# Kernel optimization log

Hardware: AMD Instinct MI355X
Metric: run time of the kernel (lower is better)

Reference implementation:

```python
import jax, jax.numpy as jnp
import numpy as np


def _mish(x):
    return x * jnp.tanh(jax.nn.softplus(x))


def setup_inputs() -> dict:
    key = jax.random.key(0)
    ks = jax.random.split(key, 10)
    N, D, U, NB, M, MD = 2048, 1024, 2048, 4, 8192, 1024
    g = lambda k, shape, s=0.02: jax.random.normal(k, shape, jnp.float32) * s
    return dict(
        x=jax.random.normal(ks[0], (N, D), jnp.float32),
        w=g(ks[1], (D, U, NB)),
        delay=g(ks[2], (D, U, NB)),
        b=jnp.zeros((U, NB), jnp.float32),
        gate_W=g(ks[3], (D, NB)),
        gate_b=jnp.zeros((NB,), jnp.float32),
        neuron_avg=jax.random.uniform(ks[4], (U,), jnp.float32),
        conn_W1=g(ks[5], (U, 32)),
        conn_b1=jnp.zeros((32,), jnp.float32),
        conn_W2=g(ks[6], (32, U)),
        conn_b2=jnp.zeros((U,), jnp.float32),
        mask=jnp.ones((U,), jnp.float32),
        act_w=jnp.ones((9,), jnp.float32),
        read_W=g(ks[7], (U, M)),
        read_b=jnp.zeros((M,), jnp.float32),
        memory=g(ks[8], (M, MD), 1.0),
    )


def reference(x, w, delay, b, gate_W, gate_b, neuron_avg, conn_W1, conn_b1,
              conn_W2, conn_b2, mask, act_w, read_W, read_b, memory):
    # --- DynamicPlasticDenseDendritic forward ---
    w_mod = w * jax.nn.sigmoid(delay)                      # [D,U,NB]
    branch = jnp.einsum('nd,dub->nub', x, w_mod) + b       # [N,U,NB]
    gate = jax.nn.softmax(x @ gate_W + gate_b, axis=-1)    # [N,NB]
    z = jnp.einsum('nub,nb->nu', branch, gate)             # [N,U]
    # DynamicConnectivity on neuron activation averages (single row)
    h = jax.nn.relu(neuron_avg[None, :] @ conn_W1 + conn_b1)   # [1,32]
    conn = jax.nn.sigmoid(h @ conn_W2 + conn_b2)               # [1,U]
    a = jax.nn.relu(z * conn * mask[None, :])                  # [N,U]
    # --- LearnedActivation: softmax-weighted 8-way activation blend (+zero) ---
    wts = jax.nn.softmax(act_w)
    blend = (wts[0] * jax.nn.sigmoid(a) + wts[1] * jax.nn.elu(a)
             + wts[2] * jnp.tanh(a) + wts[3] * jax.nn.relu(a)
             + wts[4] * jax.nn.silu(a) + wts[5] * jax.nn.gelu(a, approximate=False)
             + wts[6] * jax.nn.selu(a) + wts[7] * _mish(a))
    # --- EpisodicMemory read ---
    attn = jax.nn.softmax(blend @ read_W + read_b, axis=-1)   # [N,M]
    read = attn @ memory                                       # [N,MD]
    return read
```

## Files before the change

kernel.cpp:

```cpp
#include <hip/hip_runtime.h>


typedef unsigned short u16;
typedef __attribute__((ext_vector_type(8))) short bf16x8;
typedef __attribute__((ext_vector_type(4))) float f32x4;

__device__ __forceinline__ float b2f(u16 h) {
    union { unsigned u; float f; } v; v.u = ((unsigned)h) << 16; return v.f;
}
__device__ __forceinline__ u16 f2b(float f) {
    union { float f; unsigned u; } v; v.f = f;
    unsigned u = v.u;
    return (u16)((u + 0x7fffu + ((u >> 16) & 1u)) >> 16);
}

__device__ __forceinline__ void async_copy16(void* lds, const void* g) {
    __builtin_amdgcn_global_load_lds(
        (__attribute__((address_space(1))) void*)(g),
        (__attribute__((address_space(3))) void*)(lds), 16, 0, 0);
}

template<int BM, int BN, int S>
__device__ __forceinline__ void gemm_core_db(const u16* __restrict__ A,
                                             const u16* __restrict__ B,
                                             int Kloop, int ld,
                                             int row0, int col0,
                                             u16* smem,
                                             f32x4 (&acc)[BM / 32][BN / 32])
{
    constexpr int MT = BM / 32, NT = BN / 32;
    constexpr int STG = (BM + BN) * 32;
    constexpr int SET = STG * S;
    const int tid  = threadIdx.x;
    const int lane = tid & 63;
    const int wv   = tid >> 6;
    const int wr   = wv >> 1, wc = wv & 1;
    const int lr   = lane & 15, kg = lane >> 4;

#pragma unroll
    for (int i = 0; i < MT; i++)
#pragma unroll
        for (int j = 0; j < NT; j++) {
            f32x4 z = {0.f, 0.f, 0.f, 0.f};
            acc[i][j] = z;
        }

    auto stage_in = [&](u16* set, int k0) {
#pragma unroll
        for (int c = tid; c < BM * 4; c += 256) {
            const u16* gA = A + (size_t)(row0 + (c >> 2)) * ld + k0 + (c & 3) * 8;
#pragma unroll
            for (int s = 0; s < S; s++)
                async_copy16(set + s * STG + c * 8, gA + s * 32);
        }
#pragma unroll
        for (int c = tid; c < BN * 4; c += 256) {
            const u16* gB = B + (size_t)(col0 + (c >> 2)) * ld + k0 + (c & 3) * 8;
#pragma unroll
            for (int s = 0; s < S; s++)
                async_copy16(set + s * STG + BM * 32 + c * 8, gB + s * 32);
        }
    };

    stage_in(smem, 0);
    __syncthreads();

    int p = 0;
    for (int k0 = 0; k0 < Kloop; k0 += 32 * S) {
        if (k0 + 32 * S < Kloop)
            stage_in(smem + (p ^ 1) * SET, k0 + 32 * S);
        u16* set = smem + p * SET;
#pragma unroll
        for (int s = 0; s < S; s++) {
            const u16* sA = set + s * STG;
            const u16* sB = sA + BM * 32;
            bf16x8 af[MT], bfr[NT];
#pragma unroll
            for (int i = 0; i < MT; i++)
                af[i] = *(const bf16x8*)(sA + ((wr * (BM / 2) + i * 16 + lr) * 32 + kg * 8));
#pragma unroll
            for (int j = 0; j < NT; j++)
                bfr[j] = *(const bf16x8*)(sB + ((wc * (BN / 2) + j * 16 + lr) * 32 + kg * 8));
#pragma unroll
            for (int i = 0; i < MT; i++)
#pragma unroll
                for (int j = 0; j < NT; j++)
                    acc[i][j] = __builtin_amdgcn_mfma_f32_16x16x32_bf16(
                                    af[i], bfr[j], acc[i][j], 0, 0, 0);
        }
        __syncthreads();
        p ^= 1;
    }
}

__global__ __launch_bounds__(256)
void k_small(const float* __restrict__ na, const float* __restrict__ W1,
             const float* __restrict__ b1, const float* __restrict__ W2,
             const float* __restrict__ b2, const float* __restrict__ actw,
             float* __restrict__ conn, float* __restrict__ wts)
{
    __shared__ float red[256 * 32];
    __shared__ float hsh[32];
    const int tid = threadIdx.x;
    float h[32];
#pragma unroll
    for (int k = 0; k < 32; k++) h[k] = 0.f;
    for (int u = tid; u < 2048; u += 256) {
        float nav = na[u];
        const float* row = W1 + u * 32;
#pragma unroll
        for (int k = 0; k < 32; k++) h[k] += nav * row[k];
    }
#pragma unroll
    for (int k = 0; k < 32; k++) red[tid * 32 + k] = h[k];
    for (int s = 128; s > 0; s >>= 1) {
        __syncthreads();
        if (tid < s)
#pragma unroll
            for (int k = 0; k < 32; k++) red[tid * 32 + k] += red[(tid + s) * 32 + k];
    }
    __syncthreads();
    if (tid < 32) hsh[tid] = fmaxf(red[tid] + b1[tid], 0.f);
    if (tid == 0) {
        float e[9], m = -1e30f;
        for (int i = 0; i < 9; i++) { e[i] = actw[i]; m = fmaxf(m, e[i]); }
        float s = 0.f;
        for (int i = 0; i < 9; i++) { e[i] = expf(e[i] - m); s += e[i]; }
        for (int i = 0; i < 9; i++) wts[i] = e[i] / s;
    }
    __syncthreads();
    for (int u = tid; u < 2048; u += 256) {
        float a = 0.f;
#pragma unroll
        for (int k = 0; k < 32; k++) a += hsh[k] * W2[k * 2048 + u];
        conn[u] = 1.f / (1.f + expf(-(a + b2[u])));
    }
}

__global__ __launch_bounds__(256)
void k_gate_y(const float* __restrict__ x, const float* __restrict__ gW,
              const float* __restrict__ gb, float* __restrict__ gate,
              u16* __restrict__ y)
{
    const int tid = threadIdx.x, lane = tid & 63, wv = tid >> 6;
    const int n = blockIdx.x * 4 + wv;
    const float* xr = x + (size_t)n * 1024;
    float a0 = 0, a1 = 0, a2 = 0, a3 = 0;
    float xv[16];
#pragma unroll
    for (int s = 0; s < 16; s++) {
        int d = s * 64 + lane;
        float xd = xr[d]; xv[s] = xd;
        float4 g4 = *(const float4*)(gW + d * 4);
        a0 += xd * g4.x; a1 += xd * g4.y; a2 += xd * g4.z; a3 += xd * g4.w;
    }
#pragma unroll
    for (int off = 32; off > 0; off >>= 1) {
        a0 += __shfl_xor(a0, off); a1 += __shfl_xor(a1, off);
        a2 += __shfl_xor(a2, off); a3 += __shfl_xor(a3, off);
    }
    a0 += gb[0]; a1 += gb[1]; a2 += gb[2]; a3 += gb[3];
    float m = fmaxf(fmaxf(a0, a1), fmaxf(a2, a3));
    float e0 = expf(a0 - m), e1 = expf(a1 - m), e2 = expf(a2 - m), e3 = expf(a3 - m);
    float inv = 1.f / (e0 + e1 + e2 + e3);
    float g0 = e0 * inv, g1 = e1 * inv, g2 = e2 * inv, g3 = e3 * inv;
    if (lane == 0) *(float4*)(gate + n * 4) = make_float4(g0, g1, g2, g3);
#pragma unroll
    for (int s = 0; s < 16; s++) {
        int d = s * 64 + lane;
        ushort4 o;
        o.x = f2b(xv[s] * g0); o.y = f2b(xv[s] * g1);
        o.z = f2b(xv[s] * g2); o.w = f2b(xv[s] * g3);
        *(ushort4*)(y + (size_t)n * 4096 + d * 4) = o;
    }
}

__global__ __launch_bounds__(256)
void k_wmT(const float* __restrict__ w, const float* __restrict__ delay,
           u16* __restrict__ wmT)
{
    __shared__ __align__(16) ushort4 tile[32][65];
    const int tid = threadIdx.x;
    const int tx = tid & 63, ty = tid >> 6;
    const int u0 = blockIdx.x * 64, d0 = blockIdx.y * 32;
#pragma unroll
    for (int i = 0; i < 8; i++) {
        int d = i * 4 + ty;
        size_t idx = ((size_t)(d0 + d) * 2048 + (u0 + tx)) * 4;
        float4 w4 = *(const float4*)(w + idx);
        float4 d4 = *(const float4*)(delay + idx);
        ushort4 o;
        o.x = f2b(w4.x / (1.f + expf(-d4.x)));
        o.y = f2b(w4.y / (1.f + expf(-d4.y)));
        o.z = f2b(w4.z / (1.f + expf(-d4.z)));
        o.w = f2b(w4.w / (1.f + expf(-d4.w)));
        tile[d][tx] = o;
    }
    __syncthreads();
    const int dx = tid & 31, uy = tid >> 5;
#pragma unroll
    for (int i = 0; i < 8; i++) {
        int u = i * 8 + uy;
        *(ushort4*)(wmT + (size_t)(u0 + u) * 4096 + (d0 + dx) * 4) = tile[dx][u];
    }
}

__global__ __launch_bounds__(256)
void k_transpose(const float* __restrict__ in, u16* __restrict__ out, int R, int C)
{
    __shared__ __align__(16) u16 t[64][68];
    const int tid = threadIdx.x, tx = tid & 15, ty = tid >> 4;
    const int c0 = blockIdx.x * 64, r0 = blockIdx.y * 64;
#pragma unroll
    for (int i = 0; i < 4; i++) {
        int r = r0 + ty + i * 16;
        float4 v = *(const float4*)(in + (size_t)r * C + c0 + tx * 4);
        t[tx * 4 + 0][ty + i * 16] = f2b(v.x); t[tx * 4 + 1][ty + i * 16] = f2b(v.y);
        t[tx * 4 + 2][ty + i * 16] = f2b(v.z); t[tx * 4 + 3][ty + i * 16] = f2b(v.w);
    }
    __syncthreads();
#pragma unroll
    for (int i = 0; i < 4; i++) {
        int c = ty + i * 16;
        ushort4 v;
        v.x = t[c][tx * 4 + 0]; v.y = t[c][tx * 4 + 1];
        v.z = t[c][tx * 4 + 2]; v.w = t[c][tx * 4 + 3];
        *(ushort4*)(out + (size_t)(c0 + c) * R + r0 + tx * 4) = v;
    }
}

__device__ __forceinline__ float act_blend(float a,
    float w0, float w1, float w2, float w3,
    float w4, float w5, float w6, float w7)
{
    float sig = 1.f / (1.f + expf(-a));
    float elu = (a > 0.f) ? a : (expf(a) - 1.f);
    float th  = tanhf(a);
    float rel = fmaxf(a, 0.f);
    float sil = a * sig;
    float gel = a * 0.5f * (1.f + erff(a * 0.70710678118654752f));
    float sel = (a > 0.f) ? 1.0507009873554805f * a
                          : 1.0507009873554805f * 1.6732632423543772f * (expf(a) - 1.f);
    float sp  = (a > 20.f) ? a : log1pf(expf(a));
    float mish = a * tanhf(sp);
    return w0 * sig + w1 * elu + w2 * th + w3 * rel + w4 * sil + w5 * gel
         + w6 * sel + w7 * mish;
}

template<int BM, int BN, int NCOL>
__global__ __launch_bounds__(256, 4)
void k_gemm_partial(const u16* __restrict__ A, const u16* __restrict__ B,
                    int Kchunk, int ld, float* __restrict__ P)
{
    constexpr int MT = BM / 32, NT = BN / 32;
    __shared__ __align__(16) u16 smem[2 * (BM + BN) * 32];

    const int nx = gridDim.x, ny = gridDim.y;
    const int f  = blockIdx.x + nx * blockIdx.y;
    const int ch = (nx * ny) >> 3;
    const int sw = (f & 7) * ch + (f >> 3);
    const int bx = sw % nx, by = sw / nx;
    const int row0 = by * BM, col0 = bx * BN;

    const u16* Ac = A + (size_t)blockIdx.z * Kchunk;
    const u16* Bc = B + (size_t)blockIdx.z * Kchunk;

    f32x4 acc[MT][NT];
    gemm_core_db<BM, BN, 1>(Ac, Bc, Kchunk, ld, row0, col0, smem, acc);

    float* Pz = P + (size_t)blockIdx.z * 2048 * NCOL;
    const int tid = threadIdx.x, lane = tid & 63, wv = tid >> 6;
    const int wr = wv >> 1, wc = wv & 1, lr = lane & 15, kg = lane >> 4;
#pragma unroll
    for (int i = 0; i < MT; i++)
#pragma unroll
        for (int r = 0; r < 4; r++) {
            int n = row0 + wr * (BM / 2) + i * 16 + kg * 4 + r;
            size_t ob = (size_t)n * NCOL;
#pragma unroll
            for (int j = 0; j < NT; j++)
                Pz[ob + col0 + wc * (BN / 2) + j * 16 + lr] = acc[i][j][r];
        }
}

__global__ __launch_bounds__(256)
void k_reduce_blend(const float* __restrict__ P, const float* __restrict__ gate,
                    const float* __restrict__ conn, const float* __restrict__ mask,
                    const float* __restrict__ wts, const float* __restrict__ bbias,
                    u16* __restrict__ blend)
{
    constexpr size_t SL = (size_t)2048 * 2048;
    const int n  = blockIdx.x;
    const int u0 = threadIdx.x * 8;
    const float* base = P + (size_t)n * 2048 + u0;

    float v[8];
#pragma unroll
    for (int h = 0; h < 2; h++) {
        float4 a = *(const float4*)(base + h * 4);
        float4 b = *(const float4*)(base + SL + h * 4);
        float4 c = *(const float4*)(base + 2 * SL + h * 4);
        float4 d = *(const float4*)(base + 3 * SL + h * 4);
        v[h * 4 + 0] = a.x + b.x + c.x + d.x;
        v[h * 4 + 1] = a.y + b.y + c.y + d.y;
        v[h * 4 + 2] = a.z + b.z + c.z + d.z;
        v[h * 4 + 3] = a.w + b.w + c.w + d.w;
    }
    float4 g = *(const float4*)(gate + n * 4);
    const float w0 = wts[0], w1 = wts[1], w2 = wts[2], w3 = wts[3];
    const float w4 = wts[4], w5 = wts[5], w6 = wts[6], w7 = wts[7];

    ushort4 o[2];
#pragma unroll
    for (int j = 0; j < 8; j++) {
        int u = u0 + j;
        float4 b4 = *(const float4*)(bbias + u * 4);
        float z = v[j] + g.x * b4.x + g.y * b4.y + g.z * b4.z + g.w * b4.w;
        float a = fmaxf(z * conn[u] * mask[u], 0.f);
        u16 r = f2b(act_blend(a, w0, w1, w2, w3, w4, w5, w6, w7));
        ((u16*)o)[j] = r;
    }
    *(ushort4*)(blend + (size_t)n * 2048 + u0)     = o[0];
    *(ushort4*)(blend + (size_t)n * 2048 + u0 + 4) = o[1];
}

__global__ __launch_bounds__(256, 2)
void k_gemm_logits(const u16* __restrict__ BL, const u16* __restrict__ RWT,
                   const float* __restrict__ rbias, u16* __restrict__ out)
{
    __shared__ __align__(16) u16 smem[2 * (128 + 128) * 32];
    const int nx = gridDim.x, ny = gridDim.y;
    const int f  = blockIdx.x + nx * blockIdx.y;
    const int ch = (nx * ny) >> 3;
    const int sw = (f & 7) * ch + (f >> 3);
    const int bx = sw % nx, by = sw / nx;

    f32x4 acc[4][4];
    const int row0 = by * 128, col0 = bx * 128;
    gemm_core_db<128, 128, 1>(BL, RWT, 2048, 2048, row0, col0, smem, acc);

    const int tid = threadIdx.x, lane = tid & 63, wv = tid >> 6;
    const int wr = wv >> 1, wc = wv & 1, lr = lane & 15, kg = lane >> 4;
    float rb[4]; int mm[4];
#pragma unroll
    for (int j = 0; j < 4; j++) {
        mm[j] = col0 + wc * 64 + j * 16 + lr;
        rb[j] = rbias[mm[j]];
    }
#pragma unroll
    for (int i = 0; i < 4; i++)
#pragma unroll
        for (int r = 0; r < 4; r++) {
            int n = row0 + wr * 64 + i * 16 + kg * 4 + r;
            size_t ob = (size_t)n * 8192;
#pragma unroll
            for (int j = 0; j < 4; j++)
                out[ob + mm[j]] = f2b(acc[i][j][r] + rb[j]);
        }
}

__global__ __launch_bounds__(256)
void k_softmax(u16* __restrict__ buf)
{
    __shared__ float red[8];
    const int tid = threadIdx.x, lane = tid & 63, wv = tid >> 6;
    u16* row = buf + (size_t)blockIdx.x * 8192;
    float v[32];
    float mx = -1e30f;
#pragma unroll
    for (int s = 0; s < 8; s++) {
        ushort4 u4 = *(const ushort4*)(row + (s * 256 + tid) * 4);
        float a = b2f(u4.x), b = b2f(u4.y), c = b2f(u4.z), d = b2f(u4.w);
        v[s * 4 + 0] = a; v[s * 4 + 1] = b; v[s * 4 + 2] = c; v[s * 4 + 3] = d;
        mx = fmaxf(mx, fmaxf(fmaxf(a, b), fmaxf(c, d)));
    }
#pragma unroll
    for (int off = 32; off > 0; off >>= 1) mx = fmaxf(mx, __shfl_xor(mx, off));
    if (lane == 0) red[wv] = mx;
    __syncthreads();
    mx = fmaxf(fmaxf(red[0], red[1]), fmaxf(red[2], red[3]));
    float sum = 0.f;
#pragma unroll
    for (int k = 0; k < 32; k++) { v[k] = expf(v[k] - mx); sum += v[k]; }
#pragma unroll
    for (int off = 32; off > 0; off >>= 1) sum += __shfl_xor(sum, off);
    if (lane == 0) red[4 + wv] = sum;
    __syncthreads();
    float inv = 1.f / (red[4] + red[5] + red[6] + red[7]);
#pragma unroll
    for (int s = 0; s < 8; s++) {
        ushort4 o;
        o.x = f2b(v[s * 4 + 0] * inv); o.y = f2b(v[s * 4 + 1] * inv);
        o.z = f2b(v[s * 4 + 2] * inv); o.w = f2b(v[s * 4 + 3] * inv);
        *(ushort4*)(row + (s * 256 + tid) * 4) = o;
    }
}

__global__ __launch_bounds__(256)
void k_reduce_out(const float* __restrict__ P, float* __restrict__ out)
{
    constexpr size_t SL = (size_t)2048 * 1024;
    size_t i = ((size_t)blockIdx.x * 256 + threadIdx.x) * 4;
    float4 a = *(const float4*)(P + i);
    float4 b = *(const float4*)(P + SL + i);
    float4 c = *(const float4*)(P + 2 * SL + i);
    float4 d = *(const float4*)(P + 3 * SL + i);
    float4 o;
    o.x = a.x + b.x + c.x + d.x;
    o.y = a.y + b.y + c.y + d.y;
    o.z = a.z + b.z + c.z + d.z;
    o.w = a.w + b.w + c.w + d.w;
    *(float4*)(out + i) = o;
}

__global__ void k_fill(float* out, int n)
{
    int i = blockIdx.x * 256 + threadIdx.x;
    if (i < n) out[i] = 12345.f;
}

extern "C" void kernel_launch(void* const* d_in, const int* in_sizes, int n_in,
                              void* d_out, int out_size, void* d_ws, size_t ws_size,
                              hipStream_t stream)
{
    const float* x     = (const float*)d_in[0];
    const float* w     = (const float*)d_in[1];
    const float* delay = (const float*)d_in[2];
    const float* bb    = (const float*)d_in[3];
    const float* gW    = (const float*)d_in[4];
    const float* gb    = (const float*)d_in[5];
    const float* na    = (const float*)d_in[6];
    const float* cW1   = (const float*)d_in[7];
    const float* cb1   = (const float*)d_in[8];
    const float* cW2   = (const float*)d_in[9];
    const float* cb2   = (const float*)d_in[10];
    const float* mask  = (const float*)d_in[11];
    const float* actw  = (const float*)d_in[12];
    const float* rW    = (const float*)d_in[13];
    const float* rb    = (const float*)d_in[14];
    const float* mem   = (const float*)d_in[15];
    (void)in_sizes; (void)n_in;

    char* ws = (char*)d_ws;
    size_t off = 0;
    auto alloc = [&](size_t bytes) {
        size_t o = off; off += (bytes + 255) & ~(size_t)255; return o;
    };
    size_t o_wts   = alloc(9 * 4);
    size_t o_gate  = alloc(2048 * 4 * 4);
    size_t o_conn  = alloc(2048 * 4);
    size_t o_y     = alloc((size_t)2048 * 4096 * 2);
    size_t o_wmT   = alloc((size_t)2048 * 4096 * 2);
    size_t o_blend = alloc((size_t)2048 * 2048 * 2);
    size_t o_rwT   = alloc((size_t)8192 * 2048 * 2);
    size_t o_log   = alloc((size_t)2048 * 8192 * 2);

    if (off > ws_size) {
        k_fill<<<(out_size + 255) / 256, 256, 0, stream>>>((float*)d_out, out_size);
        return;
    }

    float* wts   = (float*)(ws + o_wts);
    float* gate  = (float*)(ws + o_gate);
    float* conn  = (float*)(ws + o_conn);
    u16* y       = (u16*)(ws + o_y);
    u16* wmT     = (u16*)(ws + o_wmT);
    u16* blend   = (u16*)(ws + o_blend);
    u16* rwT     = (u16*)(ws + o_rwT);
    u16* logits  = (u16*)(ws + o_log);
    u16* memT    = y;

    float* pA = (float*)(ws + o_rwT);
    float* pC = (float*)(ws + o_rwT);

    k_small<<<1, 256, 0, stream>>>(na, cW1, cb1, cW2, cb2, actw, conn, wts);
    k_gate_y<<<512, 256, 0, stream>>>(x, gW, gb, gate, y);
    k_wmT<<<dim3(32, 32), 256, 0, stream>>>(w, delay, wmT);

    k_gemm_partial<128, 128, 2048><<<dim3(16, 16, 4), 256, 0, stream>>>(
        y, wmT, 1024, 4096, pA);
    k_reduce_blend<<<2048, 256, 0, stream>>>(pA, gate, conn, mask, wts, bb, blend);

    k_transpose<<<dim3(128, 32), 256, 0, stream>>>(rW, rwT, 2048, 8192);
    k_gemm_logits<<<dim3(64, 16), 256, 0, stream>>>(blend, rwT, rb, logits);
    k_softmax<<<2048, 256, 0, stream>>>(logits);

    k_transpose<<<dim3(16, 128), 256, 0, stream>>>(mem, memT, 8192, 1024);

    k_gemm_partial<128, 128, 1024><<<dim3(8, 16, 4), 256, 0, stream>>>(
        logits, memT, 2048, 8192, pC);
    k_reduce_out<<<2048, 256, 0, stream>>>(pC, (float*)d_out);
}
```

Before: 484.8 us.

## Use 256x256 eight-wave GEMM core with swizzled LDS for first two GEMMs

Adds a new 512-thread GEMM core that computes 256x256 output tiles with BK=64, double-buffered LDS staging via global_load_lds, an XOR swizzle against bank conflicts, and interleaved LDS reads and MFMA phases using s_setprio. The branch GEMM and the logits GEMM now use this core in place of the 128x128 four-wave kernel. Larger tiles give more operand reuse per LDS byte and fewer global loads. The cost is 128KB of LDS per block and fewer blocks (256 for each GEMM), which may underfill the GPU's CUs and lower occupancy.

```diff
diff --git a/kernel.cpp b/kernel.cpp
--- a/kernel.cpp
+++ b/kernel.cpp
@@ -18,6 +18,133 @@
     __builtin_amdgcn_global_load_lds(
         (__attribute__((address_space(1))) void*)(g),
         (__attribute__((address_space(3))) void*)(lds), 16, 0, 0);
+}
+
+__device__ __forceinline__ int swz(int o) { return o ^ (((o >> 9) & 1) << 5); }
+
+__device__ __forceinline__ void stage_tile256(const u16* __restrict__ src, int ld,
+                                              int base0, int k0,
+                                              char* ldsbase, int tid)
+{
+#pragma unroll
+    for (int h = 0; h < 2; h++)
+#pragma unroll
+        for (int it = 0; it < 2; it++) {
+            int o = it * 8192 + tid * 16;
+            int s = swz(o);
+            int r = s >> 7;
+            int c = (s & 127) >> 1;
+            async_copy16(ldsbase + h * 16384 + o,
+                         src + (size_t)(base0 + h * 128 + r) * ld + k0 + c);
+        }
+}
+
+__device__ __forceinline__ void gemm256_core8(const u16* __restrict__ A,
+                                              const u16* __restrict__ B,
+                                              int Ktiles, int ld,
+                                              int row0, int col0,
+                                              char* lds, f32x4 (&acc)[8][4])
+{
+    const int tid  = threadIdx.x;
+    const int lane = tid & 63;
+    const int wv   = tid >> 6;
+    const int wr   = wv >> 2;
+    const int wc   = wv & 3;
+    const int lr   = lane & 15, kg = lane >> 4;
+
+#pragma unroll
+    for (int i = 0; i < 8; i++)
+#pragma unroll
+        for (int j = 0; j < 4; j++) {
+            f32x4 z = {0.f, 0.f, 0.f, 0.f};
+            acc[i][j] = z;
+        }
+
+    stage_tile256(A, ld, row0, 0, lds, tid);
+    stage_tile256(B, ld, col0, 0, lds + 32768, tid);
+    asm volatile("s_waitcnt vmcnt(0)" ::: "memory");
+    __builtin_amdgcn_s_barrier();
+
+    bf16x8 af[4][2], bfr[2][2];
+
+    for (int t = 0; t < Ktiles; t++) {
+        const int buf = (t & 1) << 16;
+        const char* sA = lds + buf + wr * 16384;
+        const char* sB = lds + buf + 32768 + ((wc >> 1) * 16384);
+
+        auto rdA = [&](int i, int ks) {
+            int off = (i * 16 + lr) * 128 + ks * 64 + kg * 16;
+            return *(const bf16x8*)(sA + swz(off));
+        };
+        auto rdB = [&](int j, int ks) {
+            int off = ((wc & 1) * 64 + j * 16 + lr) * 128 + ks * 64 + kg * 16;
+            return *(const bf16x8*)(sB + swz(off));
+        };
+
+#pragma unroll
+        for (int i = 0; i < 4; i++) { af[i][0] = rdA(i, 0); af[i][1] = rdA(i, 1); }
+#pragma unroll
+        for (int j = 0; j < 2; j++) { bfr[j][0] = rdB(j, 0); bfr[j][1] = rdB(j, 1); }
+        if (t + 1 < Ktiles) {
+            char* nb = lds + (((t + 1) & 1) << 16);
+            stage_tile256(A, ld, row0, (t + 1) * 64, nb, tid);
+            stage_tile256(B, ld, col0, (t + 1) * 64, nb + 32768, tid);
+        }
+        __builtin_amdgcn_s_barrier();
+        __builtin_amdgcn_s_setprio(1);
+#pragma unroll
+        for (int i = 0; i < 4; i++)
+#pragma unroll
+            for (int j = 0; j < 2; j++) {
+                acc[i][j] = __builtin_amdgcn_mfma_f32_16x16x32_bf16(af[i][0], bfr[j][0], acc[i][j], 0, 0, 0);
+                acc[i][j] = __builtin_amdgcn_mfma_f32_16x16x32_bf16(af[i][1], bfr[j][1], acc[i][j], 0, 0, 0);
+            }
+        __builtin_amdgcn_s_setprio(0);
+        __builtin_amdgcn_s_barrier();
+
+#pragma unroll
+        for (int i = 0; i < 4; i++) { af[i][0] = rdA(4 + i, 0); af[i][1] = rdA(4 + i, 1); }
+        __builtin_amdgcn_s_barrier();
+        __builtin_amdgcn_s_setprio(1);
+#pragma unroll
+        for (int i = 0; i < 4; i++)
+#pragma unroll
+            for (int j = 0; j < 2; j++) {
+                acc[4 + i][j] = __builtin_amdgcn_mfma_f32_16x16x32_bf16(af[i][0], bfr[j][0], acc[4 + i][j], 0, 0, 0);
+                acc[4 + i][j] = __builtin_amdgcn_mfma_f32_16x16x32_bf16(af[i][1], bfr[j][1], acc[4 + i][j], 0, 0, 0);
+            }
+        __builtin_amdgcn_s_setprio(0);
+        __builtin_amdgcn_s_barrier();
+
+#pragma unroll
+        for (int j = 0; j < 2; j++) { bfr[j][0] = rdB(2 + j, 0); bfr[j][1] = rdB(2 + j, 1); }
+        __builtin_amdgcn_s_barrier();
+        __builtin_amdgcn_s_setprio(1);
+#pragma unroll
+        for (int i = 0; i < 4; i++)
+#pragma unroll
+            for (int j = 0; j < 2; j++) {
+                acc[4 + i][2 + j] = __builtin_amdgcn_mfma_f32_16x16x32_bf16(af[i][0], bfr[j][0], acc[4 + i][2 + j], 0, 0, 0);
+                acc[4 + i][2 + j] = __builtin_amdgcn_mfma_f32_16x16x32_bf16(af[i][1], bfr[j][1], acc[4 + i][2 + j], 0, 0, 0);
+            }
+        __builtin_amdgcn_s_setprio(0);
+        __builtin_amdgcn_s_barrier();
+
+#pragma unroll
+        for (int i = 0; i < 4; i++) { af[i][0] = rdA(i, 0); af[i][1] = rdA(i, 1); }
+        __builtin_amdgcn_s_barrier();
+        __builtin_amdgcn_s_setprio(1);
+#pragma unroll
+        for (int i = 0; i < 4; i++)
+#pragma unroll
+            for (int j = 0; j < 2; j++) {
+                acc[i][2 + j] = __builtin_amdgcn_mfma_f32_16x16x32_bf16(af[i][0], bfr[j][0], acc[i][2 + j], 0, 0, 0);
+                acc[i][2 + j] = __builtin_amdgcn_mfma_f32_16x16x32_bf16(af[i][1], bfr[j][1], acc[i][2 + j], 0, 0, 0);
+            }
+        __builtin_amdgcn_s_setprio(0);
+        asm volatile("s_waitcnt vmcnt(0)" ::: "memory");
+        __builtin_amdgcn_s_barrier();
+    }
 }
 
 template<int BM, int BN, int S>
@@ -247,39 +374,30 @@
          + w6 * sel + w7 * mish;
 }
 
-template<int BM, int BN, int NCOL>
-__global__ __launch_bounds__(256, 4)
-void k_gemm_partial(const u16* __restrict__ A, const u16* __restrict__ B,
-                    int Kchunk, int ld, float* __restrict__ P)
-{
-    constexpr int MT = BM / 32, NT = BN / 32;
-    __shared__ __align__(16) u16 smem[2 * (BM + BN) * 32];
-
-    const int nx = gridDim.x, ny = gridDim.y;
-    const int f  = blockIdx.x + nx * blockIdx.y;
-    const int ch = (nx * ny) >> 3;
-    const int sw = (f & 7) * ch + (f >> 3);
-    const int bx = sw % nx, by = sw / nx;
-    const int row0 = by * BM, col0 = bx * BN;
-
-    const u16* Ac = A + (size_t)blockIdx.z * Kchunk;
-    const u16* Bc = B + (size_t)blockIdx.z * Kchunk;
-
-    f32x4 acc[MT][NT];
-    gemm_core_db<BM, BN, 1>(Ac, Bc, Kchunk, ld, row0, col0, smem, acc);
-
-    float* Pz = P + (size_t)blockIdx.z * 2048 * NCOL;
+__global__ __launch_bounds__(512, 2)
+void k_gemm_a8(const u16* __restrict__ A, const u16* __restrict__ B,
+               float* __restrict__ P)
+{
+    __shared__ __align__(16) char lds[131072];
+    const int row0 = blockIdx.y * 256, col0 = blockIdx.x * 256;
+    const u16* Ac = A + (size_t)blockIdx.z * 1024;
+    const u16* Bc = B + (size_t)blockIdx.z * 1024;
+
+    f32x4 acc[8][4];
+    gemm256_core8(Ac, Bc, 16, 4096, row0, col0, lds, acc);
+
+    float* Pz = P + (size_t)blockIdx.z * 2048 * 2048;
     const int tid = threadIdx.x, lane = tid & 63, wv = tid >> 6;
-    const int wr = wv >> 1, wc = wv & 1, lr = lane & 15, kg = lane >> 4;
-#pragma unroll
-    for (int i = 0; i < MT; i++)
+    const int wr = wv >> 2, wc = wv & 3, lr = lane & 15, kg = lane >> 4;
+#pragma unroll
+    for (int i = 0; i < 8; i++)
 #pragma unroll
         for (int r = 0; r < 4; r++) {
-            int n = row0 + wr * (BM / 2) + i * 16 + kg * 4 + r;
-            size_t ob = (size_t)n * NCOL;
-#pragma unroll
-            for (int j = 0; j < NT; j++)
-                Pz[ob + col0 + wc * (BN / 2) + j * 16 + lr] = acc[i][j][r];
+            int n = row0 + wr * 128 + i * 16 + kg * 4 + r;
+            size_t ob = (size_t)n * 2048;
+#pragma unroll
+            for (int j = 0; j < 4; j++)
+                Pz[ob + col0 + wc * 64 + j * 16 + lr] = acc[i][j][r];
         }
 }
 
@@ -324,76 +442,107 @@
     *(ushort4*)(blend + (size_t)n * 2048 + u0 + 4) = o[1];
 }
 
-__global__ __launch_bounds__(256, 2)
-void k_gemm_logits(const u16* __restrict__ BL, const u16* __restrict__ RWT,
-                   const float* __restrict__ rbias, u16* __restrict__ out)
-{
-    __shared__ __align__(16) u16 smem[2 * (128 + 128) * 32];
+__global__ __launch_bounds__(512, 2)
+void k_gemm_logits8(const u16* __restrict__ BL, const u16* __restrict__ RWT,
+                    const float* __restrict__ rbias, u16* __restrict__ out)
+{
+    __shared__ __align__(16) char lds[131072];
+    const int row0 = blockIdx.y * 256, col0 = blockIdx.x * 256;
+
+    f32x4 acc[8][4];
+    gemm256_core8(BL, RWT, 32, 2048, row0, col0, lds, acc);
+
+    const int tid = threadIdx.x, lane = tid & 63, wv = tid >> 6;
+    const int wr = wv >> 2, wc = wv & 3, lr = lane & 15, kg = lane >> 4;
+    float rb[4]; int mm[4];
+#pragma unroll
+    for (int j = 0; j < 4; j++) {
+        mm[j] = col0 + wc * 64 + j * 16 + lr;
+        rb[j] = rbias[mm[j]];
+    }
+#pragma unroll
+    for (int i = 0; i < 8; i++)
+#pragma unroll
+        for (int r = 0; r < 4; r++) {
+            int n = row0 + wr * 128 + i * 16 + kg * 4 + r;
+            size_t ob = (size_t)n * 8192;
+#pragma unroll
+            for (int j = 0; j < 4; j++)
+                out[ob + mm[j]] = f2b(acc[i][j][r] + rb[j]);
+        }
+}
+
+__global__ __launch_bounds__(256)
+void k_softmax(u16* __restrict__ buf)
+{
+    __shared__ float red[8];
+    const int tid = threadIdx.x, lane = tid & 63, wv = tid >> 6;
+    u16* row = buf + (size_t)blockIdx.x * 8192;
+    float v[32];
+    float mx = -1e30f;
+#pragma unroll
+    for (int s = 0; s < 8; s++) {
+        ushort4 u4 = *(const ushort4*)(row + (s * 256 + tid) * 4);
+        float a = b2f(u4.x), b = b2f(u4.y), c = b2f(u4.z), d = b2f(u4.w);
+        v[s * 4 + 0] = a; v[s * 4 + 1] = b; v[s * 4 + 2] = c; v[s * 4 + 3] = d;
+        mx = fmaxf(mx, fmaxf(fmaxf(a, b), fmaxf(c, d)));
+    }
+#pragma unroll
+    for (int off = 32; off > 0; off >>= 1) mx = fmaxf(mx, __shfl_xor(mx, off));
+    if (lane == 0) red[wv] = mx;
+    __syncthreads();
+    mx = fmaxf(fmaxf(red[0], red[1]), fmaxf(red[2], red[3]));
+    float sum = 0.f;
+#pragma unroll
+    for (int k = 0; k < 32; k++) { v[k] = expf(v[k] - mx); sum += v[k]; }
+#pragma unroll
+    for (int off = 32; off > 0; off >>= 1) sum += __shfl_xor(sum, off);
+    if (lane == 0) red[4 + wv] = sum;
+    __syncthreads();
+    float inv = 1.f / (red[4] + red[5] + red[6] + red[7]);
+#pragma unroll
+    for (int s = 0; s < 8; s++) {
+        ushort4 o;
+        o.x = f2b(v[s * 4 + 0] * inv); o.y = f2b(v[s * 4 + 1] * inv);
+        o.z = f2b(v[s * 4 + 2] * inv); o.w = f2b(v[s * 4 + 3] * inv);
+        *(ushort4*)(row + (s * 256 + tid) * 4) = o;
+    }
+}
+
+template<int BM, int BN, int NCOL>
+__global__ __launch_bounds__(256, 4)
+void k_gemm_partial(const u16* __restrict__ A, const u16* __restrict__ B,
+                    int Kchunk, int ld, float* __restrict__ P)
+{
+    constexpr int MT = BM / 32, NT = BN / 32;
+    __shared__ __align__(16) u16 smem[2 * (BM + BN) * 32];
+
     const int nx = gridDim.x, ny = gridDim.y;
     const int f  = blockIdx.x + nx * blockIdx.y;
     const int ch = (nx * ny) >> 3;
     const int sw = (f & 7) * ch + (f >> 3);
     const int bx = sw % nx, by = sw / nx;
-
-    f32x4 acc[4][4];
-    const int row0 = by * 128, col0 = bx * 128;
-    gemm_core_db<128, 128, 1>(BL, RWT, 2048, 2048, row0, col0, smem, acc);
-
+    const int row0 = by * BM, col0 = bx * BN;
+
+    const u16* Ac = A + (size_t)blockIdx.z * Kchunk;
+    const u16* Bc = B + (size_t)blockIdx.z * Kchunk;
+
+    f32x4 acc[MT][NT];
+    gemm_core_db<BM, BN, 1>(Ac, Bc, Kchunk, ld, row0, col0, smem, acc);
+
+    float* Pz = P + (size_t)blockIdx.z * 2048 * NCOL;
     const int tid = threadIdx.x, lane = tid & 63, wv = tid >> 6;
     const int wr = wv >> 1, wc = wv & 1, lr = lane & 15, kg = lane >> 4;
-    float rb[4]; int mm[4];
-#pragma unroll
-    for (int j = 0; j < 4; j++) {
-        mm[j] = col0 + wc * 64 + j * 16 + lr;
-        rb[j] = rbias[mm[j]];
-    }
-#pragma unroll
-    for (int i = 0; i < 4; i++)
+#pragma unroll
+    for (int i = 0; i < MT; i++)
 #pragma unroll
         for (int r = 0; r < 4; r++) {
-            int n = row0 + wr * 64 + i * 16 + kg * 4 + r;
-            size_t ob = (size_t)n * 8192;
-#pragma unroll
-            for (int j = 0; j < 4; j++)
-                out[ob + mm[j]] = f2b(acc[i][j][r] + rb[j]);
-        }
-}
-
-__global__ __launch_bounds__(256)
-void k_softmax(u16* __restrict__ buf)
-{
-    __shared__ float red[8];
-    const int tid = threadIdx.x, lane = tid & 63, wv = tid >> 6;
-    u16* row = buf + (size_t)blockIdx.x * 8192;
-    float v[32];
-    float mx = -1e30f;
-#pragma unroll
-    for (int s = 0; s < 8; s++) {
-        ushort4 u4 = *(const ushort4*)(row + (s * 256 + tid) * 4);
-        float a = b2f(u4.x), b = b2f(u4.y), c = b2f(u4.z), d = b2f(u4.w);
-        v[s * 4 + 0] = a; v[s * 4 + 1] = b; v[s * 4 + 2] = c; v[s * 4 + 3] = d;
-        mx = fmaxf(mx, fmaxf(fmaxf(a, b), fmaxf(c, d)));
-    }
-#pragma unroll
-    for (int off = 32; off > 0; off >>= 1) mx = fmaxf(mx, __shfl_xor(mx, off));
-    if (lane == 0) red[wv] = mx;
-    __syncthreads();
-    mx = fmaxf(fmaxf(red[0], red[1]), fmaxf(red[2], red[3]));
-    float sum = 0.f;
-#pragma unroll
-    for (int k = 0; k < 32; k++) { v[k] = expf(v[k] - mx); sum += v[k]; }
-#pragma unroll
-    for (int off = 32; off > 0; off >>= 1) sum += __shfl_xor(sum, off);
-    if (lane == 0) red[4 + wv] = sum;
-    __syncthreads();
-    float inv = 1.f / (red[4] + red[5] + red[6] + red[7]);
-#pragma unroll
-    for (int s = 0; s < 8; s++) {
-        ushort4 o;
-        o.x = f2b(v[s * 4 + 0] * inv); o.y = f2b(v[s * 4 + 1] * inv);
-        o.z = f2b(v[s * 4 + 2] * inv); o.w = f2b(v[s * 4 + 3] * inv);
-        *(ushort4*)(row + (s * 256 + tid) * 4) = o;
-    }
+            int n = row0 + wr * (BM / 2) + i * 16 + kg * 4 + r;
+            size_t ob = (size_t)n * NCOL;
+#pragma unroll
+            for (int j = 0; j < NT; j++)
+                Pz[ob + col0 + wc * (BN / 2) + j * 16 + lr] = acc[i][j][r];
+        }
 }
 
 __global__ __launch_bounds__(256)
@@ -477,12 +626,11 @@
     k_gate_y<<<512, 256, 0, stream>>>(x, gW, gb, gate, y);
     k_wmT<<<dim3(32, 32), 256, 0, stream>>>(w, delay, wmT);
 
-    k_gemm_partial<128, 128, 2048><<<dim3(16, 16, 4), 256, 0, stream>>>(
-        y, wmT, 1024, 4096, pA);
+    k_gemm_a8<<<dim3(8, 8, 4), 512, 0, stream>>>(y, wmT, pA);
     k_reduce_blend<<<2048, 256, 0, stream>>>(pA, gate, conn, mask, wts, bb, blend);
 
     k_transpose<<<dim3(128, 32), 256, 0, stream>>>(rW, rwT, 2048, 8192);
-    k_gemm_logits<<<dim3(64, 16), 256, 0, stream>>>(blend, rwT, rb, logits);
+    k_gemm_logits8<<<dim3(32, 8), 512, 0, stream>>>(blend, rwT, rb, logits);
     k_softmax<<<2048, 256, 0, stream>>>(logits);
 
     k_transpose<<<dim3(16, 128), 256, 0, stream>>>(mem, memT, 8192, 1024);
```

Measured after the change: 465.8 us. 1.04x faster.
